# Optimization experiments

Measured on AMD Instinct MI355X. Metric: run time of the kernel, lower is better.

The kernel has to match this reference:

```python
import jax, jax.numpy as jnp
import numpy as np

INP_DIM, EMB_DIM, NUM_HEADS = 2048, 512, 2
LAMBDA_ATTN = 10.0
BS, L = 16, 1024


def _l2norm(x, axis=-1, eps=1e-12):
    # matches torch F.normalize: x / max(||x||, eps)
    n = jnp.sqrt(jnp.sum(x * x, axis=axis, keepdims=True))
    return x / jnp.maximum(n, eps)


def setup_inputs() -> dict:
    key = jax.random.key(0)
    k1, k2, kw, kb = jax.random.split(key, 4)
    img1 = jax.random.normal(k1, (BS, INP_DIM, L), dtype=jnp.float32)
    img2 = jax.random.normal(k2, (BS, INP_DIM, L), dtype=jnp.float32)
    # per-head query projection weights, stacked: (H, inp_dim, emb_dim)
    lim = 1.0 / np.sqrt(INP_DIM)
    W = jax.random.uniform(kw, (NUM_HEADS, INP_DIM, EMB_DIM), jnp.float32, -lim, lim)
    b = jax.random.uniform(kb, (NUM_HEADS, EMB_DIM), jnp.float32, -lim, lim)
    return {"img1": img1, "img2": img2, "W": W, "b": b}


def reference(img1, img2, W, b):
    # img1, img2: (bs, inp_dim, L) -> (bs, L, inp_dim)
    x1 = jnp.swapaxes(img1, 1, 2)
    x2 = jnp.swapaxes(img2, 1, 2)
    # per-head query projections: (H, bs, L, emb)
    q1 = jnp.einsum('bld,hde->hble', x1, W) + b[:, None, None, :]
    q2 = jnp.einsum('bld,hde->hble', x2, W) + b[:, None, None, :]
    # cosine relevance (attn_normalized=True): (H, bs, L, L)
    n1 = _l2norm(q1)
    n2 = _l2norm(q2)
    rel = jnp.einsum('hble,hbme->hblm', n1, n2) * LAMBDA_ATTN
    row_attn = jax.nn.softmax(rel, axis=3)  # softmax over img2 positions (dim=2 in torch)
    col_attn = jax.nn.softmax(rel, axis=2)  # softmax over img1 positions (dim=1 in torch)
    sim12 = row_attn.sum(axis=2)  # (H, bs, L) -> weight on img2 positions
    sim21 = col_attn.sum(axis=3)  # (H, bs, L) -> weight on img1 positions
    sim12 = sim12 / (sim12.sum(axis=-1, keepdims=True) + 1e-8)
    sim21 = sim21 / (sim21.sum(axis=-1, keepdims=True) + 1e-8)
    # torch module returns lists sim_in_img1 (=sim21) and sim_in_img2 (=sim12);
    # stack them: (2, H, bs, L)
    return jnp.stack([sim21, sim12], axis=0)
```

## Files before the change

### kernel.cpp

```cpp
#include <hip/hip_runtime.h>
#include <cstdint>
#include <cstddef>

#define INP 2048
#define EMB 512
#define NHEAD 2
#define BSZ 16
#define SEQ 1024
#define LAMBDA 10.0f

typedef __attribute__((ext_vector_type(8))) short bf16x8;
typedef __attribute__((ext_vector_type(16))) float f32x16;

__device__ __forceinline__ short f2bf(float x) {
    union { float f; unsigned u; } v; v.f = x;
    unsigned r = v.u + 0x7fffu + ((v.u >> 16) & 1u);
    return (short)(r >> 16);
}
__device__ __forceinline__ float bf2f(short h) {
    union { unsigned u; float f; } v; v.u = ((unsigned)(unsigned short)h) << 16;
    return v.f;
}
__device__ __forceinline__ void g2lds16(const void* g, void* l) {
    __builtin_amdgcn_global_load_lds(
        (const __attribute__((address_space(1))) unsigned int*)g,
        (__attribute__((address_space(3))) unsigned int*)l, 16, 0, 0);
}

__global__ __launch_bounds__(256) void zero_kernel(float* __restrict__ p, int n) {
    int i = blockIdx.x * 256 + threadIdx.x;
    if (i < n) p[i] = 0.f;
}

__global__ __launch_bounds__(256) void conv_t(const float* __restrict__ src,
                                              short* __restrict__ hi, int L) {
    const int l0 = blockIdx.x * 64;
    const int d0 = blockIdx.y * 32;
    const float* s = src + (size_t)blockIdx.z * INP * L;

    __shared__ float tl[32][65];
    const int t  = threadIdx.x;
    const int dr = t >> 3;
    const int f4 = (t & 7) * 4;

    float4 v0 = *(const float4*)&s[(size_t)(d0 + dr) * L + l0 + f4];
    float4 v1 = *(const float4*)&s[(size_t)(d0 + dr) * L + l0 + f4 + 32];
    tl[dr][f4 + 0] = v0.x; tl[dr][f4 + 1] = v0.y; tl[dr][f4 + 2] = v0.z; tl[dr][f4 + 3] = v0.w;
    tl[dr][f4 + 32] = v1.x; tl[dr][f4 + 33] = v1.y; tl[dr][f4 + 34] = v1.z; tl[dr][f4 + 35] = v1.w;
    __syncthreads();

    const int kgl = t >> 6;
    const int l   = t & 63;
    bf16x8 hv8;
#pragma unroll
    for (int q = 0; q < 8; q++) hv8[q] = f2bf(tl[kgl * 8 + q][l]);
    const size_t slot = (size_t)blockIdx.z * (INP / 8) * L
                      + (size_t)(blockIdx.y * 4 + kgl) * L + l0 + l;
    *(bf16x8*)&hi[slot * 8] = hv8;
}

__global__ __launch_bounds__(256) void proj_mfma(
    const short* __restrict__ Ahg, const short* __restrict__ Bhg,
    const float* __restrict__ bias, float* __restrict__ Q, int im, int bbase) {
    const int bid = blockIdx.x;
    const int xcd = bid & 7;
    const int s   = bid >> 3;
    const int zl  = xcd * 2 + (s >> 5);
    const int t2  = s & 31;
    const int et  = t2 & 3;
    const int lt  = t2 >> 2;
    const int l0 = lt * 128;
    const int e0 = et * 128;
    const int h    = zl >> 3;
    const int bloc = zl & 7;
    const int z = (im * NHEAD + h) * BSZ + bbase + bloc;

    const short* __restrict__ Ah = Ahg + (size_t)bloc * SEQ * INP;
    const short* __restrict__ Bh = Bhg + (size_t)h * EMB * INP;

    __shared__ short sA[4096], sB[4096];

    const int tid  = threadIdx.x;
    const int lane = tid & 63;
    const int wid  = tid >> 6;
    const int wm = (wid & 1) * 64;
    const int wn = (wid >> 1) * 64;
    const int fm = lane & 31;
    const int khl = lane >> 5;

    const short* gB = (wid & 2) ? Bh : Ah;
    short* lB = (wid & 2) ? sB : sA;
    const int ps = (wid & 2) ? EMB : SEQ;
    const int rb = (wid & 2) ? e0 : l0;
    const int gb = (wid & 1) * 2;

    f32x16 acc[2][2];
#pragma unroll
    for (int i = 0; i < 2; i++)
#pragma unroll
        for (int j = 0; j < 2; j++)
#pragma unroll
            for (int r = 0; r < 16; r++) acc[i][j][r] = 0.f;

    for (int k0 = 0; k0 < INP; k0 += 32) {
        const int k08 = k0 >> 3;
        __syncthreads();
#pragma unroll
        for (int v = 0; v < 4; v++) {
            const int g = gb + (v >> 1), hh = v & 1;
            g2lds16(gB + ((size_t)(k08 + g) * ps + rb + hh * 64 + lane) * 8,
                    lB + (g * 128 + hh * 64) * 8);
        }
        __syncthreads();

        bf16x8 afh[2][2], bfh[2][2];
#pragma unroll
        for (int i = 0; i < 2; i++)
#pragma unroll
            for (int ks = 0; ks < 2; ks++) {
                const int ra = ((ks * 2 + khl) * 128 + wm + i * 32 + fm) * 8;
                afh[i][ks] = *(const bf16x8*)&sA[ra];
                const int rbi = ((ks * 2 + khl) * 128 + wn + i * 32 + fm) * 8;
                bfh[i][ks] = *(const bf16x8*)&sB[rbi];
            }
#pragma unroll
        for (int ks = 0; ks < 2; ks++)
#pragma unroll
            for (int i = 0; i < 2; i++)
#pragma unroll
                for (int j = 0; j < 2; j++)
                    acc[i][j] = __builtin_amdgcn_mfma_f32_32x32x16_bf16(afh[i][ks], bfh[j][ks], acc[i][j], 0, 0, 0);
    }

    float* __restrict__ Qz = Q + (size_t)z * SEQ * EMB;
    float bj[2];
#pragma unroll
    for (int j = 0; j < 2; j++) bj[j] = bias[h * EMB + e0 + wn + j * 32 + fm];
    const int rhalf = khl * 4;
#pragma unroll
    for (int i = 0; i < 2; i++)
#pragma unroll
        for (int r = 0; r < 16; r++) {
            const int row = l0 + wm + i * 32 + (r & 3) + 8 * (r >> 2) + rhalf;
#pragma unroll
            for (int j = 0; j < 2; j++) {
                const int col = e0 + wn + j * 32 + fm;
                Qz[(size_t)row * EMB + col] = acc[i][j][r] + bj[j];
            }
        }
}

__global__ __launch_bounds__(256) void norm_split(const float* __restrict__ Q,
                                                  short* __restrict__ Qhi) {
    const int z  = blockIdx.y;
    const int r0 = blockIdx.x * 4;
    const int t  = threadIdx.x;
    const int w    = t >> 6;
    const int lane = t & 63;
    const float* p = Q + ((size_t)z * SEQ + r0 + w) * EMB;

    float4 a = *(const float4*)&p[lane * 8];
    float4 b = *(const float4*)&p[lane * 8 + 4];
    float sq = a.x * a.x + a.y * a.y + a.z * a.z + a.w * a.w
             + b.x * b.x + b.y * b.y + b.z * b.z + b.w * b.w;
#pragma unroll
    for (int o = 32; o > 0; o >>= 1) sq += __shfl_xor(sq, o);
    float scale = 1.f / fmaxf(sqrtf(sq), 1e-12f);
    if (z < NHEAD * BSZ) scale *= LAMBDA;

    float v[8] = {a.x * scale, a.y * scale, a.z * scale, a.w * scale,
                  b.x * scale, b.y * scale, b.z * scale, b.w * scale};
    bf16x8 hv8;
#pragma unroll
    for (int q = 0; q < 8; q++) hv8[q] = f2bf(v[q]);
    __shared__ short shi[64 * 4 * 8];
    *(bf16x8*)&shi[(lane * 4 + w) * 8] = hv8;
    __syncthreads();

    const int kg = t >> 2, rl = t & 3;
    const size_t dst = ((size_t)z * (EMB / 8) + kg) * SEQ + r0 + rl;
    *(bf16x8*)&Qhi[dst * 8] = *(const bf16x8*)&shi[t * 8];
}

__global__ __launch_bounds__(256) void attn_mfma(
    const short* __restrict__ Qhi,
    short* __restrict__ E, float* __restrict__ Zr, float* __restrict__ Zc) {
    const int bid = blockIdx.x;
    const int xcd = bid & 7;
    const int s   = bid >> 3;
    const int hb  = xcd * 4 + (s >> 6);
    const int t   = s & 63;
    const int lt  = t & 7;
    const int mt  = t >> 3;
    const int l0 = lt * 128;
    const int m0 = mt * 128;

    const short* __restrict__ Ah = Qhi + (size_t)hb * SEQ * EMB;
    const short* __restrict__ Bh = Qhi + (size_t)(NHEAD * BSZ + hb) * SEQ * EMB;

    __shared__ short sA[4096], sB[4096];
    __shared__ float redR[128], redC[128];

    const int tid  = threadIdx.x;
    const int lane = tid & 63;
    const int wid  = tid >> 6;
    const int wm = (wid & 1) * 64;
    const int wn = (wid >> 1) * 64;
    const int fm = lane & 31;
    const int khl = lane >> 5;

    const short* gB = (wid & 2) ? Bh : Ah;
    short* lB = (wid & 2) ? sB : sA;
    const int rb = (wid & 2) ? m0 : l0;
    const int gb = (wid & 1) * 2;

    f32x16 acc[2][2];
#pragma unroll
    for (int i = 0; i < 2; i++)
#pragma unroll
        for (int j = 0; j < 2; j++)
#pragma unroll
            for (int r = 0; r < 16; r++) acc[i][j][r] = 0.f;

    for (int k0 = 0; k0 < EMB; k0 += 32) {
        const int k08 = k0 >> 3;
        __syncthreads();
#pragma unroll
        for (int v = 0; v < 4; v++) {
            const int g = gb + (v >> 1), hh = v & 1;
            g2lds16(gB + ((size_t)(k08 + g) * SEQ + rb + hh * 64 + lane) * 8,
                    lB + (g * 128 + hh * 64) * 8);
        }
        __syncthreads();

        bf16x8 afh[2][2], bfh[2][2];
#pragma unroll
        for (int i = 0; i < 2; i++)
#pragma unroll
            for (int ks = 0; ks < 2; ks++) {
                const int ra = ((ks * 2 + khl) * 128 + wm + i * 32 + fm) * 8;
                afh[i][ks] = *(const bf16x8*)&sA[ra];
                const int rbi = ((ks * 2 + khl) * 128 + wn + i * 32 + fm) * 8;
                bfh[i][ks] = *(const bf16x8*)&sB[rbi];
            }
#pragma unroll
        for (int ks = 0; ks < 2; ks++)
#pragma unroll
            for (int i = 0; i < 2; i++)
#pragma unroll
                for (int j = 0; j < 2; j++)
                    acc[i][j] = __builtin_amdgcn_mfma_f32_32x32x16_bf16(afh[i][ks], bfh[j][ks], acc[i][j], 0, 0, 0);
    }

    if (tid < 128) { redR[tid] = 0.f; redC[tid] = 0.f; }
    __syncthreads();

    short* __restrict__ Ez = E + (size_t)hb * SEQ * SEQ;
    const int rhalf = khl * 4;
    float cj0 = 0.f, cj1 = 0.f;
#pragma unroll
    for (int i = 0; i < 2; i++)
#pragma unroll
        for (int r = 0; r < 16; r++) {
            const int row = wm + i * 32 + (r & 3) + 8 * (r >> 2) + rhalf;
            const short e0s = f2bf(expf(acc[i][0][r]));
            const short e1s = f2bf(expf(acc[i][1][r]));
            const float e0v = bf2f(e0s);
            const float e1v = bf2f(e1s);
            Ez[(size_t)(l0 + row) * SEQ + m0 + wn + fm]      = e0s;
            Ez[(size_t)(l0 + row) * SEQ + m0 + wn + 32 + fm] = e1s;
            float rv = e0v + e1v;
#pragma unroll
            for (int o = 16; o > 0; o >>= 1) rv += __shfl_xor(rv, o);
            if ((lane & 31) == 0) atomicAdd(&redR[row], rv);
            cj0 += e0v; cj1 += e1v;
        }
    cj0 += __shfl_xor(cj0, 32);
    cj1 += __shfl_xor(cj1, 32);
    if (lane < 32) {
        atomicAdd(&redC[wn + fm], cj0);
        atomicAdd(&redC[wn + 32 + fm], cj1);
    }
    __syncthreads();

    if (tid < 128) {
        atomicAdd(&Zr[hb * SEQ + l0 + tid], redR[tid]);
        atomicAdd(&Zc[hb * SEQ + m0 + tid], redC[tid]);
    }
}

__global__ __launch_bounds__(256) void reduce_pass(
    const short* __restrict__ E, const float* __restrict__ Zr,
    const float* __restrict__ Zc, float* __restrict__ S21, float* __restrict__ S12) {
    const int lblk = blockIdx.x;
    const int hb   = blockIdx.y;
    const int tid  = threadIdx.x;
    const int lane = tid & 63;
    const int wid  = tid >> 6;
    const short* __restrict__ Ez = E + (size_t)hb * SEQ * SEQ;

    __shared__ float colred[SEQ];
    for (int i = tid; i < SEQ; i += 256) colred[i] = 0.f;
    __syncthreads();

    float izc[2][8];
#pragma unroll
    for (int it = 0; it < 2; it++)
#pragma unroll
        for (int q = 0; q < 8; q++)
            izc[it][q] = 1.f / Zc[hb * SEQ + it * 512 + lane * 8 + q];

    float colacc[2][8];
#pragma unroll
    for (int it = 0; it < 2; it++)
#pragma unroll
        for (int q = 0; q < 8; q++) colacc[it][q] = 0.f;

    for (int rr = 0; rr < 32; rr++) {
        const int row = lblk * 128 + wid * 32 + rr;
        const float izr = 1.f / Zr[hb * SEQ + row];
        float rowsum = 0.f;
#pragma unroll
        for (int it = 0; it < 2; it++) {
            bf16x8 ev = *(const bf16x8*)&Ez[(size_t)row * SEQ + it * 512 + lane * 8];
#pragma unroll
            for (int q = 0; q < 8; q++) {
                const float e = bf2f(ev[q]);
                rowsum += e * izc[it][q];
                colacc[it][q] += e * izr;
            }
        }
#pragma unroll
        for (int o = 32; o > 0; o >>= 1) rowsum += __shfl_down(rowsum, o);
        if (lane == 0) S21[hb * SEQ + row] = rowsum;
    }
#pragma unroll
    for (int it = 0; it < 2; it++)
#pragma unroll
        for (int q = 0; q < 8; q++)
            atomicAdd(&colred[it * 512 + lane * 8 + q], colacc[it][q]);
    __syncthreads();
    for (int i = tid; i < SEQ; i += 256) atomicAdd(&S12[hb * SEQ + i], colred[i]);
}

__global__ __launch_bounds__(256) void fin_kernel(
    const float* __restrict__ S21, const float* __restrict__ S12,
    float* __restrict__ out) {
    const int z  = blockIdx.x;
    const int w  = z / (NHEAD * BSZ);
    const int hb = z % (NHEAD * BSZ);
    const float* __restrict__ src = (w == 0 ? S21 : S12) + (size_t)hb * SEQ;
    const int t = threadIdx.x;

    float s = 0.f;
    for (int i = t; i < SEQ; i += 256) s += src[i];
#pragma unroll
    for (int o = 32; o > 0; o >>= 1) s += __shfl_down(s, o);
    __shared__ float red[4];
    if ((t & 63) == 0) red[t >> 6] = s;
    __syncthreads();
    const float total = red[0] + red[1] + red[2] + red[3];
    const float inv = 1.f / (total + 1e-8f);
    for (int i = t; i < SEQ; i += 256)
        out[(size_t)z * SEQ + i] = src[i] * inv;
}

extern "C" void kernel_launch(void* const* d_in, const int* in_sizes, int n_in,
                              void* d_out, int out_size, void* d_ws, size_t ws_size,
                              hipStream_t stream) {
    const float* img1 = (const float*)d_in[0];
    const float* img2 = (const float*)d_in[1];
    const float* W    = (const float*)d_in[2];
    const float* bias = (const float*)d_in[3];
    float* out = (float*)d_out;

    const size_t QN = (size_t)2 * NHEAD * BSZ * SEQ * EMB;
    const size_t WN = (size_t)NHEAD * EMB * INP;
    const size_t CN = (size_t)8 * SEQ * INP;

    short* Qhi = (short*)d_ws;
    short* Wth = Qhi + QN;
    short* iTh = Wth + WN;
    float* Q   = (float*)(iTh + CN);
    short* E   = (short*)Q;
    float* Zr  = Q + QN;
    float* Zc  = Zr + (size_t)NHEAD * BSZ * SEQ;
    float* S21 = Zc + (size_t)NHEAD * BSZ * SEQ;
    float* S12 = S21 + (size_t)NHEAD * BSZ * SEQ;

    zero_kernel<<<dim3(512), dim3(256), 0, stream>>>(Zr, 4 * NHEAD * BSZ * SEQ);

    conv_t<<<dim3(EMB / 64, INP / 32, NHEAD), dim3(256), 0, stream>>>(W, Wth, EMB);

    for (int c = 0; c < 4; c++) {
        const int im = c >> 1;
        const int bbase = (c & 1) * 8;
        const float* img = (im == 0 ? img1 : img2) + (size_t)bbase * INP * SEQ;
        conv_t<<<dim3(SEQ / 64, INP / 32, 8), dim3(256), 0, stream>>>(img, iTh, SEQ);
        proj_mfma<<<dim3(512), dim3(256), 0, stream>>>(
            iTh, Wth, bias, Q, im, bbase);
    }

    norm_split<<<dim3(SEQ / 4, 2 * NHEAD * BSZ), dim3(256), 0, stream>>>(Q, Qhi);

    attn_mfma<<<dim3(2048), dim3(256), 0, stream>>>(Qhi, E, Zr, Zc);

    reduce_pass<<<dim3(8, NHEAD * BSZ), dim3(256), 0, stream>>>(E, Zr, Zc, S21, S12);

    fin_kernel<<<dim3(2 * NHEAD * BSZ), dim3(256), 0, stream>>>(S21, S12, out);
    (void)in_sizes; (void)n_in; (void)out_size; (void)ws_size;
}
```

Baseline: 622.1 us.

## Fuse projection with L2 normalization and double-buffer full-row GEMM tiles

```diff
diff --git a/kernel.cpp b/kernel.cpp
--- a/kernel.cpp
+++ b/kernel.cpp
@@ -59,127 +59,145 @@
     *(bf16x8*)&hi[slot * 8] = hv8;
 }
 
-__global__ __launch_bounds__(256) void proj_mfma(
-    const short* __restrict__ Ahg, const short* __restrict__ Bhg,
-    const float* __restrict__ bias, float* __restrict__ Q, int im, int bbase) {
+__global__ __launch_bounds__(512, 2) void proj_norm(
+    const short* __restrict__ iT, const short* __restrict__ Wt,
+    const float* __restrict__ bias, short* __restrict__ Qhi) {
     const int bid = blockIdx.x;
     const int xcd = bid & 7;
     const int s   = bid >> 3;
-    const int zl  = xcd * 2 + (s >> 5);
-    const int t2  = s & 31;
-    const int et  = t2 & 3;
-    const int lt  = t2 >> 2;
-    const int l0 = lt * 128;
-    const int e0 = et * 128;
-    const int h    = zl >> 3;
-    const int bloc = zl & 7;
-    const int z = (im * NHEAD + h) * BSZ + bbase + bloc;
-
-    const short* __restrict__ Ah = Ahg + (size_t)bloc * SEQ * INP;
-    const short* __restrict__ Bh = Bhg + (size_t)h * EMB * INP;
-
-    __shared__ short sA[4096], sB[4096];
+    const int zh  = s >> 3;
+    const int lt  = s & 7;
+    const int pair = xcd * 8 + zh;
+    const int slab = pair >> 1;
+    const int h    = pair & 1;
+    const int im   = slab >> 4;
+    const int b    = slab & 15;
+    const int zo   = (im * 2 + h) * 16 + b;
+    const int l0   = lt * 128;
+
+    const short* __restrict__ Ag = iT + (size_t)slab * (INP / 8) * SEQ * 8;
+    const short* __restrict__ Bg = Wt + (size_t)h * (INP / 8) * EMB * 8;
+
+    __shared__ short sA[2][4096];
+    __shared__ short sB[2][16384];
+    __shared__ float sRed[128];
 
     const int tid  = threadIdx.x;
     const int lane = tid & 63;
     const int wid  = tid >> 6;
-    const int wm = (wid & 1) * 64;
-    const int wn = (wid >> 1) * 64;
-    const int fm = lane & 31;
-    const int khl = lane >> 5;
-
-    const short* gB = (wid & 2) ? Bh : Ah;
-    short* lB = (wid & 2) ? sB : sA;
-    const int ps = (wid & 2) ? EMB : SEQ;
-    const int rb = (wid & 2) ? e0 : l0;
-    const int gb = (wid & 1) * 2;
-
-    f32x16 acc[2][2];
+    const int wr   = wid >> 2;
+    const int wc   = wid & 3;
+    const int fm   = lane & 31;
+    const int khl  = lane >> 5;
+
+    if (tid < 128) sRed[tid] = 0.f;
+
+    float bj[4];
+#pragma unroll
+    for (int j = 0; j < 4; j++) bj[j] = bias[h * EMB + wc * 128 + j * 32 + fm];
+
+    f32x16 acc[2][4];
 #pragma unroll
     for (int i = 0; i < 2; i++)
 #pragma unroll
-        for (int j = 0; j < 2; j++)
+        for (int j = 0; j < 4; j++)
 #pragma unroll
             for (int r = 0; r < 16; r++) acc[i][j][r] = 0.f;
 
-    for (int k0 = 0; k0 < INP; k0 += 32) {
-        const int k08 = k0 >> 3;
-        __syncthreads();
-#pragma unroll
-        for (int v = 0; v < 4; v++) {
-            const int g = gb + (v >> 1), hh = v & 1;
-            g2lds16(gB + ((size_t)(k08 + g) * ps + rb + hh * 64 + lane) * 8,
-                    lB + (g * 128 + hh * 64) * 8);
-        }
-        __syncthreads();
-
-        bf16x8 afh[2][2], bfh[2][2];
+    const int gA = wid >> 1;
+    const int rA = (wid & 1) * 64;
+
+    {
+        g2lds16(Ag + ((size_t)gA * SEQ + l0 + rA + lane) * 8,
+                &sA[0][(wid * 64) * 8]);
+#pragma unroll
+        for (int c = 0; c < 4; c++)
+            g2lds16(Bg + ((size_t)c * EMB + wid * 64 + lane) * 8,
+                    &sB[0][(c * 512 + wid * 64) * 8]);
+    }
+    asm volatile("s_waitcnt vmcnt(0)" ::: "memory");
+    __builtin_amdgcn_s_barrier();
+
+    for (int kt = 0; kt < INP / 32; kt++) {
+        const int cur = kt & 1;
+        if (kt + 1 < INP / 32) {
+            const int k08 = (kt + 1) * 4;
+            const int nb  = cur ^ 1;
+            g2lds16(Ag + ((size_t)(k08 + gA) * SEQ + l0 + rA + lane) * 8,
+                    &sA[nb][(wid * 64) * 8]);
+#pragma unroll
+            for (int c = 0; c < 4; c++)
+                g2lds16(Bg + ((size_t)(k08 + c) * EMB + wid * 64 + lane) * 8,
+                        &sB[nb][(c * 512 + wid * 64) * 8]);
+        }
+        asm volatile("s_waitcnt vmcnt(5)" ::: "memory");
+
+        bf16x8 af[2][2], bf[4][2];
+#pragma unroll
+        for (int ks = 0; ks < 2; ks++) {
+#pragma unroll
+            for (int i = 0; i < 2; i++)
+                af[i][ks] = *(const bf16x8*)&sA[cur][((ks * 2 + khl) * 128 + wr * 64 + i * 32 + fm) * 8];
+#pragma unroll
+            for (int j = 0; j < 4; j++)
+                bf[j][ks] = *(const bf16x8*)&sB[cur][((ks * 2 + khl) * 512 + wc * 128 + j * 32 + fm) * 8];
+        }
+#pragma unroll
+        for (int ks = 0; ks < 2; ks++)
+#pragma unroll
+            for (int i = 0; i < 2; i++)
+#pragma unroll
+                for (int j = 0; j < 4; j++)
+                    acc[i][j] = __builtin_amdgcn_mfma_f32_32x32x16_bf16(af[i][ks], bf[j][ks], acc[i][j], 0, 0, 0);
+        __builtin_amdgcn_s_barrier();
+    }
+
+#pragma unroll
+    for (int i = 0; i < 2; i++)
+#pragma unroll
+        for (int r = 0; r < 16; r++) {
+            float ssq = 0.f;
+#pragma unroll
+            for (int j = 0; j < 4; j++) {
+                acc[i][j][r] += bj[j];
+                ssq += acc[i][j][r] * acc[i][j][r];
+            }
+#pragma unroll
+            for (int o = 1; o < 32; o <<= 1) ssq += __shfl_xor(ssq, o);
+            if (fm == 0)
+                atomicAdd(&sRed[wr * 64 + i * 32 + (r & 3) + 8 * (r >> 2) + khl * 4], ssq);
+        }
+    asm volatile("s_waitcnt lgkmcnt(0)" ::: "memory");
+    __builtin_amdgcn_s_barrier();
+
+    const float lam = (im == 0) ? LAMBDA : 1.f;
+#pragma unroll
+    for (int i = 0; i < 2; i++)
+#pragma unroll
+        for (int r = 0; r < 16; r++) {
+            const int rloc = i * 32 + (r & 3) + 8 * (r >> 2) + khl * 4;
+            const float sc = lam / fmaxf(sqrtf(sRed[wr * 64 + rloc]), 1e-12f);
+#pragma unroll
+            for (int j = 0; j < 4; j++) acc[i][j][r] *= sc;
+        }
+
+    short* scr = &sB[0][0] + wid * 2048;
+#pragma unroll
+    for (int j = 0; j < 4; j++) {
 #pragma unroll
         for (int i = 0; i < 2; i++)
 #pragma unroll
-            for (int ks = 0; ks < 2; ks++) {
-                const int ra = ((ks * 2 + khl) * 128 + wm + i * 32 + fm) * 8;
-                afh[i][ks] = *(const bf16x8*)&sA[ra];
-                const int rbi = ((ks * 2 + khl) * 128 + wn + i * 32 + fm) * 8;
-                bfh[i][ks] = *(const bf16x8*)&sB[rbi];
+            for (int r = 0; r < 16; r++) {
+                const int rloc = i * 32 + (r & 3) + 8 * (r >> 2) + khl * 4;
+                scr[((fm >> 3) * 64 + rloc) * 8 + (fm & 7)] = f2bf(acc[i][j][r]);
             }
 #pragma unroll
-        for (int ks = 0; ks < 2; ks++)
-#pragma unroll
-            for (int i = 0; i < 2; i++)
-#pragma unroll
-                for (int j = 0; j < 2; j++)
-                    acc[i][j] = __builtin_amdgcn_mfma_f32_32x32x16_bf16(afh[i][ks], bfh[j][ks], acc[i][j], 0, 0, 0);
-    }
-
-    float* __restrict__ Qz = Q + (size_t)z * SEQ * EMB;
-    float bj[2];
-#pragma unroll
-    for (int j = 0; j < 2; j++) bj[j] = bias[h * EMB + e0 + wn + j * 32 + fm];
-    const int rhalf = khl * 4;
-#pragma unroll
-    for (int i = 0; i < 2; i++)
-#pragma unroll
-        for (int r = 0; r < 16; r++) {
-            const int row = l0 + wm + i * 32 + (r & 3) + 8 * (r >> 2) + rhalf;
-#pragma unroll
-            for (int j = 0; j < 2; j++) {
-                const int col = e0 + wn + j * 32 + fm;
-                Qz[(size_t)row * EMB + col] = acc[i][j][r] + bj[j];
-            }
-        }
-}
-
-__global__ __launch_bounds__(256) void norm_split(const float* __restrict__ Q,
-                                                  short* __restrict__ Qhi) {
-    const int z  = blockIdx.y;
-    const int r0 = blockIdx.x * 4;
-    const int t  = threadIdx.x;
-    const int w    = t >> 6;
-    const int lane = t & 63;
-    const float* p = Q + ((size_t)z * SEQ + r0 + w) * EMB;
-
-    float4 a = *(const float4*)&p[lane * 8];
-    float4 b = *(const float4*)&p[lane * 8 + 4];
-    float sq = a.x * a.x + a.y * a.y + a.z * a.z + a.w * a.w
-             + b.x * b.x + b.y * b.y + b.z * b.z + b.w * b.w;
-#pragma unroll
-    for (int o = 32; o > 0; o >>= 1) sq += __shfl_xor(sq, o);
-    float scale = 1.f / fmaxf(sqrtf(sq), 1e-12f);
-    if (z < NHEAD * BSZ) scale *= LAMBDA;
-
-    float v[8] = {a.x * scale, a.y * scale, a.z * scale, a.w * scale,
-                  b.x * scale, b.y * scale, b.z * scale, b.w * scale};
-    bf16x8 hv8;
-#pragma unroll
-    for (int q = 0; q < 8; q++) hv8[q] = f2bf(v[q]);
-    __shared__ short shi[64 * 4 * 8];
-    *(bf16x8*)&shi[(lane * 4 + w) * 8] = hv8;
-    __syncthreads();
-
-    const int kg = t >> 2, rl = t & 3;
-    const size_t dst = ((size_t)z * (EMB / 8) + kg) * SEQ + r0 + rl;
-    *(bf16x8*)&Qhi[dst * 8] = *(const bf16x8*)&shi[t * 8];
+        for (int k = 0; k < 4; k++) {
+            bf16x8 vv = *(const bf16x8*)&scr[(k * 64 + lane) * 8];
+            const int kg = zo * 64 + wc * 16 + j * 4 + k;
+            *(bf16x8*)&Qhi[((size_t)kg * 1024 + l0 + wr * 64 + lane) * 8] = vv;
+        }
+    }
 }
 
 __global__ __launch_bounds__(256) void attn_mfma(
@@ -374,16 +392,16 @@
     const float* bias = (const float*)d_in[3];
     float* out = (float*)d_out;
 
-    const size_t QN = (size_t)2 * NHEAD * BSZ * SEQ * EMB;
-    const size_t WN = (size_t)NHEAD * EMB * INP;
-    const size_t CN = (size_t)8 * SEQ * INP;
+    const size_t QN  = (size_t)2 * NHEAD * BSZ * SEQ * EMB;
+    const size_t WN  = (size_t)NHEAD * EMB * INP;
+    const size_t CNF = (size_t)32 * SEQ * INP;
+    const size_t EN  = (size_t)NHEAD * BSZ * SEQ * SEQ;
 
     short* Qhi = (short*)d_ws;
     short* Wth = Qhi + QN;
     short* iTh = Wth + WN;
-    float* Q   = (float*)(iTh + CN);
-    short* E   = (short*)Q;
-    float* Zr  = Q + QN;
+    short* E   = iTh + CNF;
+    float* Zr  = (float*)(E + EN);
     float* Zc  = Zr + (size_t)NHEAD * BSZ * SEQ;
     float* S21 = Zc + (size_t)NHEAD * BSZ * SEQ;
     float* S12 = S21 + (size_t)NHEAD * BSZ * SEQ;
@@ -392,16 +410,11 @@
 
     conv_t<<<dim3(EMB / 64, INP / 32, NHEAD), dim3(256), 0, stream>>>(W, Wth, EMB);
 
-    for (int c = 0; c < 4; c++) {
-        const int im = c >> 1;
-        const int bbase = (c & 1) * 8;
-        const float* img = (im == 0 ? img1 : img2) + (size_t)bbase * INP * SEQ;
-        conv_t<<<dim3(SEQ / 64, INP / 32, 8), dim3(256), 0, stream>>>(img, iTh, SEQ);
-        proj_mfma<<<dim3(512), dim3(256), 0, stream>>>(
-            iTh, Wth, bias, Q, im, bbase);
-    }
-
-    norm_split<<<dim3(SEQ / 4, 2 * NHEAD * BSZ), dim3(256), 0, stream>>>(Q, Qhi);
+    conv_t<<<dim3(SEQ / 64, INP / 32, 16), dim3(256), 0, stream>>>(img1, iTh, SEQ);
+    conv_t<<<dim3(SEQ / 64, INP / 32, 16), dim3(256), 0, stream>>>(
+        img2, iTh + (size_t)16 * (INP / 8) * SEQ * 8, SEQ);
+
+    proj_norm<<<dim3(512), dim3(512), 0, stream>>>(iTh, Wth, bias, Qhi);
 
     attn_mfma<<<dim3(2048), dim3(256), 0, stream>>>(Qhi, E, Zr, Zc);
 
```

New measurement: 603.7 us. -3.0%, faster.

## Merge projection into one 256x256-tile GEMM with 4-stage LDS prefetch pipeline

Applied to the files above, without the earlier changes.

```diff
diff --git a/kernel.cpp b/kernel.cpp
--- a/kernel.cpp
+++ b/kernel.cpp
@@ -59,94 +59,114 @@
     *(bf16x8*)&hi[slot * 8] = hv8;
 }
 
-__global__ __launch_bounds__(256) void proj_mfma(
-    const short* __restrict__ Ahg, const short* __restrict__ Bhg,
-    const float* __restrict__ bias, float* __restrict__ Q, int im, int bbase) {
+__global__ __launch_bounds__(512, 2) void proj_gemm(
+    const short* __restrict__ iT, const short* __restrict__ Wt,
+    const float* __restrict__ bias, float* __restrict__ Q) {
     const int bid = blockIdx.x;
     const int xcd = bid & 7;
     const int s   = bid >> 3;
-    const int zl  = xcd * 2 + (s >> 5);
-    const int t2  = s & 31;
-    const int et  = t2 & 3;
-    const int lt  = t2 >> 2;
-    const int l0 = lt * 128;
-    const int e0 = et * 128;
-    const int h    = zl >> 3;
-    const int bloc = zl & 7;
-    const int z = (im * NHEAD + h) * BSZ + bbase + bloc;
-
-    const short* __restrict__ Ah = Ahg + (size_t)bloc * SEQ * INP;
-    const short* __restrict__ Bh = Bhg + (size_t)h * EMB * INP;
-
-    __shared__ short sA[4096], sB[4096];
+    const int g   = s >> 2;
+    const int v   = s & 3;
+    const int h   = v >> 1;
+    const int nh  = v & 1;
+    const int gg  = xcd * 16 + g;
+    const int slab  = gg >> 2;
+    const int mtile = gg & 3;
+    const int mb = mtile * 256;
+    const int nb = nh * 256;
+    const int im = slab >> 4;
+    const int b  = slab & 15;
+    const int z  = (im * 2 + h) * 16 + b;
+
+    const short* __restrict__ Ag = iT + (size_t)slab * (INP / 8) * SEQ * 8;
+    const short* __restrict__ Bg = Wt + (size_t)h * (INP / 8) * EMB * 8;
+
+    __shared__ short sL[4][16384];
 
     const int tid  = threadIdx.x;
     const int lane = tid & 63;
     const int wid  = tid >> 6;
-    const int wm = (wid & 1) * 64;
-    const int wn = (wid >> 1) * 64;
-    const int fm = lane & 31;
-    const int khl = lane >> 5;
-
-    const short* gB = (wid & 2) ? Bh : Ah;
-    short* lB = (wid & 2) ? sB : sA;
-    const int ps = (wid & 2) ? EMB : SEQ;
-    const int rb = (wid & 2) ? e0 : l0;
-    const int gb = (wid & 1) * 2;
-
-    f32x16 acc[2][2];
-#pragma unroll
-    for (int i = 0; i < 2; i++)
+    const int wm   = (wid >> 2) * 128;
+    const int wn   = (wid & 3) * 64;
+    const int fm   = lane & 31;
+    const int khl  = lane >> 5;
+
+    const int sgp = wid >> 2;
+    const int srq = wid & 3;
+
+    float bj[2];
+#pragma unroll
+    for (int j = 0; j < 2; j++) bj[j] = bias[h * EMB + nb + wn + j * 32 + fm];
+    asm volatile("s_waitcnt vmcnt(0)" ::: "memory");
+
+#define STAGE(tt) { \
+    const int k8_ = (tt) * 4; \
+    short* bA_ = &sL[(tt) & 3][0]; \
+    short* bB_ = &sL[(tt) & 3][8192]; \
+    g2lds16(Ag + ((size_t)(k8_ + sgp) * SEQ + mb + srq * 64 + lane) * 8, \
+            bA_ + (sgp * 256 + srq * 64) * 8); \
+    g2lds16(Ag + ((size_t)(k8_ + sgp + 2) * SEQ + mb + srq * 64 + lane) * 8, \
+            bA_ + ((sgp + 2) * 256 + srq * 64) * 8); \
+    g2lds16(Bg + ((size_t)(k8_ + sgp) * EMB + nb + srq * 64 + lane) * 8, \
+            bB_ + (sgp * 256 + srq * 64) * 8); \
+    g2lds16(Bg + ((size_t)(k8_ + sgp + 2) * EMB + nb + srq * 64 + lane) * 8, \
+            bB_ + ((sgp + 2) * 256 + srq * 64) * 8); \
+}
+
+    f32x16 acc[4][2];
+#pragma unroll
+    for (int i = 0; i < 4; i++)
 #pragma unroll
         for (int j = 0; j < 2; j++)
 #pragma unroll
             for (int r = 0; r < 16; r++) acc[i][j][r] = 0.f;
 
-    for (int k0 = 0; k0 < INP; k0 += 32) {
-        const int k08 = k0 >> 3;
-        __syncthreads();
-#pragma unroll
-        for (int v = 0; v < 4; v++) {
-            const int g = gb + (v >> 1), hh = v & 1;
-            g2lds16(gB + ((size_t)(k08 + g) * ps + rb + hh * 64 + lane) * 8,
-                    lB + (g * 128 + hh * 64) * 8);
+    STAGE(0);
+    STAGE(1);
+    asm volatile("s_waitcnt vmcnt(4)" ::: "memory");
+    __builtin_amdgcn_s_barrier();
+
+    for (int t = 0; t < 64; t++) {
+        if (t < 62) STAGE(t + 2);
+
+        const short* bA = &sL[t & 3][0];
+        const short* bB = &sL[t & 3][8192];
+        bf16x8 af[4][2], bf[2][2];
+#pragma unroll
+        for (int ks = 0; ks < 2; ks++) {
+            const int pl = (ks * 2 + khl) * 256;
+#pragma unroll
+            for (int i = 0; i < 4; i++)
+                af[i][ks] = *(const bf16x8*)&bA[(pl + wm + i * 32 + fm) * 8];
+#pragma unroll
+            for (int j = 0; j < 2; j++)
+                bf[j][ks] = *(const bf16x8*)&bB[(pl + wn + j * 32 + fm) * 8];
         }
-        __syncthreads();
-
-        bf16x8 afh[2][2], bfh[2][2];
-#pragma unroll
-        for (int i = 0; i < 2; i++)
-#pragma unroll
-            for (int ks = 0; ks < 2; ks++) {
-                const int ra = ((ks * 2 + khl) * 128 + wm + i * 32 + fm) * 8;
-                afh[i][ks] = *(const bf16x8*)&sA[ra];
-                const int rbi = ((ks * 2 + khl) * 128 + wn + i * 32 + fm) * 8;
-                bfh[i][ks] = *(const bf16x8*)&sB[rbi];
-            }
+        __builtin_amdgcn_s_setprio(1);
 #pragma unroll
         for (int ks = 0; ks < 2; ks++)
 #pragma unroll
-            for (int i = 0; i < 2; i++)
+            for (int i = 0; i < 4; i++)
 #pragma unroll
                 for (int j = 0; j < 2; j++)
-                    acc[i][j] = __builtin_amdgcn_mfma_f32_32x32x16_bf16(afh[i][ks], bfh[j][ks], acc[i][j], 0, 0, 0);
+                    acc[i][j] = __builtin_amdgcn_mfma_f32_32x32x16_bf16(af[i][ks], bf[j][ks], acc[i][j], 0, 0, 0);
+        __builtin_amdgcn_s_setprio(0);
+
+        if (t < 62)       asm volatile("s_waitcnt vmcnt(4)" ::: "memory");
+        else if (t == 62) asm volatile("s_waitcnt vmcnt(0)" ::: "memory");
+        if (t < 63) __builtin_amdgcn_s_barrier();
     }
+#undef STAGE
 
     float* __restrict__ Qz = Q + (size_t)z * SEQ * EMB;
-    float bj[2];
-#pragma unroll
-    for (int j = 0; j < 2; j++) bj[j] = bias[h * EMB + e0 + wn + j * 32 + fm];
-    const int rhalf = khl * 4;
-#pragma unroll
-    for (int i = 0; i < 2; i++)
+#pragma unroll
+    for (int i = 0; i < 4; i++)
 #pragma unroll
         for (int r = 0; r < 16; r++) {
-            const int row = l0 + wm + i * 32 + (r & 3) + 8 * (r >> 2) + rhalf;
-#pragma unroll
-            for (int j = 0; j < 2; j++) {
-                const int col = e0 + wn + j * 32 + fm;
-                Qz[(size_t)row * EMB + col] = acc[i][j][r] + bj[j];
-            }
+            const int row = mb + wm + i * 32 + (r & 3) + 8 * (r >> 2) + khl * 4;
+#pragma unroll
+            for (int j = 0; j < 2; j++)
+                Qz[(size_t)row * EMB + nb + wn + j * 32 + fm] = acc[i][j][r] + bj[j];
         }
 }
 
@@ -374,14 +394,14 @@
     const float* bias = (const float*)d_in[3];
     float* out = (float*)d_out;
 
-    const size_t QN = (size_t)2 * NHEAD * BSZ * SEQ * EMB;
-    const size_t WN = (size_t)NHEAD * EMB * INP;
-    const size_t CN = (size_t)8 * SEQ * INP;
+    const size_t QN  = (size_t)2 * NHEAD * BSZ * SEQ * EMB;
+    const size_t WN  = (size_t)NHEAD * EMB * INP;
+    const size_t CNF = (size_t)32 * SEQ * INP;
 
     short* Qhi = (short*)d_ws;
     short* Wth = Qhi + QN;
     short* iTh = Wth + WN;
-    float* Q   = (float*)(iTh + CN);
+    float* Q   = (float*)(iTh + CNF);
     short* E   = (short*)Q;
     float* Zr  = Q + QN;
     float* Zc  = Zr + (size_t)NHEAD * BSZ * SEQ;
@@ -392,14 +412,11 @@
 
     conv_t<<<dim3(EMB / 64, INP / 32, NHEAD), dim3(256), 0, stream>>>(W, Wth, EMB);
 
-    for (int c = 0; c < 4; c++) {
-        const int im = c >> 1;
-        const int bbase = (c & 1) * 8;
-        const float* img = (im == 0 ? img1 : img2) + (size_t)bbase * INP * SEQ;
-        conv_t<<<dim3(SEQ / 64, INP / 32, 8), dim3(256), 0, stream>>>(img, iTh, SEQ);
-        proj_mfma<<<dim3(512), dim3(256), 0, stream>>>(
-            iTh, Wth, bias, Q, im, bbase);
-    }
+    conv_t<<<dim3(SEQ / 64, INP / 32, 16), dim3(256), 0, stream>>>(img1, iTh, SEQ);
+    conv_t<<<dim3(SEQ / 64, INP / 32, 16), dim3(256), 0, stream>>>(
+        img2, iTh + (size_t)16 * (INP / 8) * SEQ * 8, SEQ);
+
+    proj_gemm<<<dim3(512), dim3(512), 0, stream>>>(iTh, Wth, bias, Q);
 
     norm_split<<<dim3(SEQ / 4, 2 * NHEAD * BSZ), dim3(256), 0, stream>>>(Q, Qhi);
 
```

After: 555.8 us. 1.12x faster.
